# Optimization experiments

Measured on AMD Instinct MI355X. Metric: run time of the kernel, lower is better.

Reference implementation:

```python
import jax, jax.numpy as jnp
import numpy as np

B, T, D = 4, 2048, 1024
H, K, V, S, C = 8, 128, 128, 512, 256
R = T // C
W = 2 * C
TAU = float(K) ** 0.5
NEG = 1e30  # INFTY_APPROX from source


def rel_shift(x):
    # Transformer-XL relative shift; x: [B,H,R,C,W]
    lead = x.shape[:-2]
    c, w = x.shape[-2:]
    x = jnp.pad(x, [(0, 0)] * (x.ndim - 1) + [(1, 0)])
    x = x.reshape(*lead, w + 1, c)
    return x[..., 1:, :].reshape(*lead, c, w)


def setup_inputs():
    key = jax.random.key(0)
    ks = jax.random.split(key, 9)
    sd = lambda n: 1.0 / np.sqrt(n)
    f32 = jnp.float32
    return dict(
        x=jax.random.normal(ks[0], (B, T, D), f32),
        g_ln=jnp.ones((D,), f32),
        Wq=jax.random.normal(ks[1], (D, H, K), f32) * sd(D),
        Wk=jax.random.normal(ks[2], (D, H, K), f32) * sd(D),
        Wv=jax.random.normal(ks[3], (D, H, V), f32) * sd(D),
        codebook=jax.random.normal(ks[4], (H, S, K), f32),
        xl_r=jax.random.normal(ks[5], (H, W, K), f32) * sd(D),
        xl_u=jax.random.normal(ks[6], (H, K), f32) * 0.02,
        xl_v=jax.random.normal(ks[7], (H, K), f32) * 0.02,
        Wo=jax.random.normal(ks[8], (H, V, D), f32) * sd(H * V),
    )


def reference(x, g_ln, Wq, Wk, Wv, codebook, xl_r, xl_u, xl_v, Wo):
    # RMSNorm
    xt = x * jax.lax.rsqrt(jnp.mean(jnp.square(x), axis=-1, keepdims=True) + 1e-6) * g_ln
    # QKV projections, reshaped to blocks: [B,H,R,C,*]
    q = jnp.einsum('btd,dhk->bhtk', xt, Wq).reshape(B, H, R, C, K)
    k = jnp.einsum('btd,dhk->bhtk', xt, Wk).reshape(B, H, R, C, K)
    v = jnp.einsum('btd,dhv->bhtv', xt, Wv).reshape(B, H, R, C, V)
    # VQ codebook assignment (per-head nearest codeword)
    d2 = (jnp.sum(k * k, -1, keepdims=True)
          - 2.0 * jnp.einsum('bhrck,hsk->bhrcs', k, codebook)
          + jnp.sum(codebook * codebook, -1)[None, :, None, None, :])
    z = jnp.argmin(d2, axis=-1)                      # shortcodes [B,H,R,C]
    delta = jax.nn.one_hot(z, S, dtype=k.dtype)      # [B,H,R,C,S]
    k_hat_q = jnp.einsum('bhrcs,hsk->bhrck', delta, codebook)
    k_hat = k + jax.lax.stop_gradient(k_hat_q - k)   # straight-through quantized keys
    # causal cumulative per-code cluster stats ('matmul' reduction from source)
    d1 = jnp.sum(delta, axis=3)                      # counts per block [B,H,R,S]
    d1c = jnp.cumsum(d1, axis=2)
    fracs = jnp.tril(jnp.einsum('bhrs,bhgs->bhsrg', 1.0 / jnp.clip(d1c, 1.0), d1))
    lower = jnp.pad(d1c[:, :, :-2], ((0, 0), (0, 0), (2, 0), (0, 0)))
    dv = jnp.einsum('bhrcs,bhrcv->bhrsv', delta, v)
    dvn = dv / jnp.clip(d1[..., None], 1.0)
    dvnc = jnp.einsum('bhsrg,bhgsv->bhrsv', fracs, dvn)
    upper_div_lower = jnp.pad(dvnc[:, :, :-2], ((0, 0), (0, 0), (2, 0), (0, 0), (0, 0)))
    # attention over recent window (prev+current block) and codebook cache
    q_u = q + xl_u[None, :, None, None, :]
    q_v = q + xl_v[None, :, None, None, :]
    k_hat_prev = jnp.pad(k_hat[:, :, :-1], ((0, 0), (0, 0), (1, 0), (0, 0), (0, 0)))
    v_prev = jnp.pad(v[:, :, :-1], ((0, 0), (0, 0), (1, 0), (0, 0), (0, 0)))
    k_recent = jnp.concatenate([k_hat_prev, k_hat], axis=3)  # [B,H,R,W,K]
    v_recent = jnp.concatenate([v_prev, v], axis=3)          # [B,H,R,W,V]
    ac = jnp.einsum('bhrck,bhrwk->bhrcw', q_u, k_recent)
    bd = rel_shift(jnp.einsum('bhrck,hwk->bhrcw', q_v, xl_r))
    recent = (ac + bd) / TAU
    i = jnp.arange(C)[:, None]
    j = jnp.arange(W)[None, :]
    causal = j <= i + C                                            # [C,W]
    first = (jnp.arange(R)[:, None, None] == 0) & (j[None] < C)    # mask zero-padded prev of block 0
    mask = causal[None] & jnp.logical_not(first)                   # [R,C,W]
    recent = jnp.where(mask[None, None], recent, -NEG)
    cache = jnp.einsum('bhrck,hsk->bhrcs', q_u, codebook) / TAU
    cache = cache + jnp.where(lower > 0, jnp.log(jnp.maximum(lower, 1.0)), -NEG)[:, :, :, None, :]
    attn = jax.nn.softmax(jnp.concatenate([cache, recent], axis=-1), axis=-1)
    out = (jnp.einsum('bhrcs,bhrsv->bhrcv', attn[..., :S], upper_div_lower)
           + jnp.einsum('bhrcw,bhrwv->bhrcv', attn[..., S:], v_recent))
    res = jnp.einsum('bhtv,hvd->btd', out.reshape(B, H, T, V), Wo)
    return res
```

## Files before the change

### kernel.cpp

```cpp
#include <hip/hip_runtime.h>
#include <hip/hip_fp16.h>

typedef _Float16 half8 __attribute__((ext_vector_type(8)));
typedef float f32x4 __attribute__((ext_vector_type(4)));

constexpr int Bn = 4, Tn = 2048, Dn = 1024, Hn = 8, Kn = 128, Vn = 128;
constexpr int Sn = 512, Cn = 256, Rn = 8, Wn = 512;
constexpr float NEGV = 1.0e30f;
constexpr float INV_TAU = 0.08838834764831845f;

__device__ __forceinline__ half8 ldh8(const __half* p) {
  return *reinterpret_cast<const half8*>(p);
}
__device__ __forceinline__ void sth8(__half* p, half8 v) {
  *reinterpret_cast<half8*>(p) = v;
}
__device__ __forceinline__ f32x4 mfma16(half8 a, half8 b, f32x4 c) {
  return __builtin_amdgcn_mfma_f32_16x16x32_f16(a, b, c, 0, 0, 0);
}

__global__ __launch_bounds__(256) void rms3_k(const float* __restrict__ x,
                                              const float* __restrict__ g,
                                              __half* __restrict__ xth,
                                              __half* __restrict__ xtl) {
  const int row = blockIdx.x;
  const int tid = threadIdx.x;
  const float4 v = reinterpret_cast<const float4*>(x + (size_t)row * Dn)[tid];
  float ss = v.x * v.x + v.y * v.y + v.z * v.z + v.w * v.w;
#pragma unroll
  for (int o = 32; o > 0; o >>= 1) ss += __shfl_xor(ss, o);
  __shared__ float red[4];
  if ((tid & 63) == 0) red[tid >> 6] = ss;
  __syncthreads();
  const float tot = red[0] + red[1] + red[2] + red[3];
  const float sc = rsqrtf(tot * (1.0f / Dn) + 1e-6f);
  const float4 gv = reinterpret_cast<const float4*>(g)[tid];
  float vv[4] = {v.x * sc * gv.x, v.y * sc * gv.y, v.z * sc * gv.z,
                 v.w * sc * gv.w};
  __half hi[4], lo[4];
#pragma unroll
  for (int e = 0; e < 4; ++e) {
    hi[e] = __float2half(vv[e]);
    lo[e] = __float2half(vv[e] - __half2float(hi[e]));
  }
  __half2* oph = reinterpret_cast<__half2*>(xth + (size_t)row * Dn + tid * 4);
  __half2* opl = reinterpret_cast<__half2*>(xtl + (size_t)row * Dn + tid * 4);
  oph[0] = __halves2half2(hi[0], hi[1]);
  oph[1] = __halves2half2(hi[2], hi[3]);
  opl[0] = __halves2half2(lo[0], lo[1]);
  opl[1] = __halves2half2(lo[2], lo[3]);
}

__global__ __launch_bounds__(256) void transcvt_k(const float* __restrict__ src,
                                                  __half* __restrict__ dst) {
  __shared__ float ts[32][33];
  const int bx = blockIdx.x, by = blockIdx.y;
  const int j = threadIdx.x & 31, i0 = threadIdx.x >> 5;
#pragma unroll
  for (int rr = 0; rr < 4; ++rr) {
    const int row = i0 + rr * 8;
    ts[row][j] = src[(size_t)(by * 32 + row) * 1024 + bx * 32 + j];
  }
  __syncthreads();
#pragma unroll
  for (int rr = 0; rr < 4; ++rr) {
    const int row = i0 + rr * 8;
    dst[(size_t)(bx * 32 + row) * 1024 + by * 32 + j] = __float2half(ts[j][row]);
  }
}

__global__ __launch_bounds__(256) void transcvt2_k(
    const float* __restrict__ src, __half* __restrict__ dh,
    __half* __restrict__ dl) {
  __shared__ float ts[32][33];
  const int bx = blockIdx.x, by = blockIdx.y;
  const int j = threadIdx.x & 31, i0 = threadIdx.x >> 5;
#pragma unroll
  for (int rr = 0; rr < 4; ++rr) {
    const int row = i0 + rr * 8;
    ts[row][j] = src[(size_t)(by * 32 + row) * 1024 + bx * 32 + j];
  }
  __syncthreads();
#pragma unroll
  for (int rr = 0; rr < 4; ++rr) {
    const int row = i0 + rr * 8;
    const float v = ts[j][row];
    const __half hi = __float2half(v);
    dh[(size_t)(bx * 32 + row) * 1024 + by * 32 + j] = hi;
    dl[(size_t)(bx * 32 + row) * 1024 + by * 32 + j] =
        __float2half(v - __half2float(hi));
  }
}

__global__ __launch_bounds__(256) void cb2_k(const float* __restrict__ cb,
                                             float* __restrict__ cb2v) {
  const int idx = blockIdx.x * 256 + threadIdx.x;
  const float4* rp = reinterpret_cast<const float4*>(cb + (size_t)idx * Kn);
  float ss = 0.f;
#pragma unroll 8
  for (int i = 0; i < Kn / 4; ++i) {
    const float4 v = rp[i];
    ss += v.x * v.x + v.y * v.y + v.z * v.z + v.w * v.w;
  }
  cb2v[idx] = ss;
}

__global__ __launch_bounds__(256) void cvt2_k(const float* __restrict__ cb,
                                              const float* __restrict__ xlr,
                                              __half* __restrict__ cbh,
                                              __half* __restrict__ cbl,
                                              __half* __restrict__ xlrh) {
  const int i = blockIdx.x * 256 + threadIdx.x;
  constexpr int NE = Hn * Sn * Kn;
  if (i < NE) {
    const float v = cb[i];
    const __half hi = __float2half(v);
    cbh[i] = hi;
    cbl[i] = __float2half(v - __half2float(hi));
  } else {
    xlrh[i - NE] = __float2half(xlr[i - NE]);
  }
}

__global__ __launch_bounds__(256) void duv_k(const float* __restrict__ xlr,
                                             const float* __restrict__ xlu,
                                             const float* __restrict__ xlv,
                                             float* __restrict__ duv) {
  const int h = blockIdx.x;
  const float* up = xlu + h * Kn;
  const float* vp = xlv + h * Kn;
  for (int j = threadIdx.x; j < Wn; j += 256) {
    const float* rp = xlr + ((size_t)h * Wn + j) * Kn;
    float s = 0.f;
#pragma unroll 8
    for (int d = 0; d < Kn; ++d) s = fmaf(vp[d] - up[d], rp[d], s);
    duv[h * Wn + j] = s;
  }
}

__global__ __launch_bounds__(256, 2) void kproj_k(
    const __half* __restrict__ Ah, const __half* __restrict__ Al,
    const __half* __restrict__ Bh, const __half* __restrict__ Bl,
    __half* __restrict__ Ch, __half* __restrict__ Cl, int M, int KD) {
  __shared__ __half AsH[128 * 72];
  __shared__ __half AsL[128 * 72];
  __shared__ __half BsH[128 * 72];
  __shared__ __half BsL[128 * 72];
  const int tid = threadIdx.x;
  const int lane = tid & 63, wq = tid >> 6;
  const int lrow = lane & 15, lk8 = (lane >> 4) << 3;
  const int m0 = blockIdx.x * 128, n0 = blockIdx.y * 128;
  const int srow = tid >> 2, spart = tid & 3;

  f32x4 acc[2][8];
#pragma unroll
  for (int mt = 0; mt < 2; ++mt)
#pragma unroll
    for (int nt = 0; nt < 8; ++nt) acc[mt][nt] = (f32x4){0.f, 0.f, 0.f, 0.f};

  for (int kt = 0; kt < KD; kt += 64) {
    __syncthreads();
#pragma unroll
    for (int hh = 0; hh < 2; ++hh) {
      const int row = srow + hh * 64;
      const size_t ao = (size_t)(m0 + row) * KD + kt + spart * 16;
      const size_t bo = (size_t)(n0 + row) * KD + kt + spart * 16;
      sth8(&AsH[row * 72 + spart * 16], ldh8(Ah + ao));
      sth8(&AsH[row * 72 + spart * 16 + 8], ldh8(Ah + ao + 8));
      sth8(&AsL[row * 72 + spart * 16], ldh8(Al + ao));
      sth8(&AsL[row * 72 + spart * 16 + 8], ldh8(Al + ao + 8));
      sth8(&BsH[row * 72 + spart * 16], ldh8(Bh + bo));
      sth8(&BsH[row * 72 + spart * 16 + 8], ldh8(Bh + bo + 8));
      sth8(&BsL[row * 72 + spart * 16], ldh8(Bl + bo));
      sth8(&BsL[row * 72 + spart * 16 + 8], ldh8(Bl + bo + 8));
    }
    __syncthreads();
#pragma unroll
    for (int ks = 0; ks < 2; ++ks) {
      const half8 a0h = ldh8(&AsH[(32 * wq + lrow) * 72 + lk8 + 32 * ks]);
      const half8 a1h = ldh8(&AsH[(32 * wq + 16 + lrow) * 72 + lk8 + 32 * ks]);
      const half8 a0l = ldh8(&AsL[(32 * wq + lrow) * 72 + lk8 + 32 * ks]);
      const half8 a1l = ldh8(&AsL[(32 * wq + 16 + lrow) * 72 + lk8 + 32 * ks]);
#pragma unroll
      for (int nt = 0; nt < 8; ++nt) {
        const half8 bh = ldh8(&BsH[(16 * nt + lrow) * 72 + lk8 + 32 * ks]);
        const half8 bl = ldh8(&BsL[(16 * nt + lrow) * 72 + lk8 + 32 * ks]);
        acc[0][nt] = mfma16(a0h, bh, acc[0][nt]);
        acc[0][nt] = mfma16(a0h, bl, acc[0][nt]);
        acc[0][nt] = mfma16(a0l, bh, acc[0][nt]);
        acc[1][nt] = mfma16(a1h, bh, acc[1][nt]);
        acc[1][nt] = mfma16(a1h, bl, acc[1][nt]);
        acc[1][nt] = mfma16(a1l, bh, acc[1][nt]);
      }
    }
  }
  __half* OH = Ch + (size_t)(n0 >> 7) * M * 128;
  __half* OL = Cl + (size_t)(n0 >> 7) * M * 128;
#pragma unroll
  for (int mt = 0; mt < 2; ++mt)
#pragma unroll
    for (int nt = 0; nt < 8; ++nt)
#pragma unroll
      for (int reg = 0; reg < 4; ++reg) {
        const int row = m0 + 32 * wq + 16 * mt + 4 * (lane >> 4) + reg;
        const float v = acc[mt][nt][reg];
        const __half hi = __float2half(v);
        OH[(size_t)row * 128 + 16 * nt + lrow] = hi;
        OL[(size_t)row * 128 + 16 * nt + lrow] =
            __float2half(v - __half2float(hi));
      }
}

template <int MODE>
__global__ __launch_bounds__(256, 4) void gemmh_k(const __half* __restrict__ A,
                                                  const __half* __restrict__ Bt,
                                                  void* __restrict__ Cout,
                                                  int M, int N, int KD) {
  __shared__ __half As[128 * 72];
  __shared__ __half Bs[128 * 72];
  const int tid = threadIdx.x;
  const int lane = tid & 63, wq = tid >> 6;
  const int lrow = lane & 15, lk8 = (lane >> 4) << 3;
  const int m0 = blockIdx.x * 128, n0 = blockIdx.y * 128;
  const int srow = tid >> 2, spart = tid & 3;

  f32x4 acc[2][8];
#pragma unroll
  for (int mt = 0; mt < 2; ++mt)
#pragma unroll
    for (int nt = 0; nt < 8; ++nt) acc[mt][nt] = (f32x4){0.f, 0.f, 0.f, 0.f};

  for (int kt = 0; kt < KD; kt += 64) {
    __syncthreads();
#pragma unroll
    for (int hh = 0; hh < 2; ++hh) {
      const int row = srow + hh * 64;
      const __half* pa = A + (size_t)(m0 + row) * KD + kt + spart * 16;
      const __half* pb = Bt + (size_t)(n0 + row) * KD + kt + spart * 16;
      sth8(&As[row * 72 + spart * 16], ldh8(pa));
      sth8(&As[row * 72 + spart * 16 + 8], ldh8(pa + 8));
      sth8(&Bs[row * 72 + spart * 16], ldh8(pb));
      sth8(&Bs[row * 72 + spart * 16 + 8], ldh8(pb + 8));
    }
    __syncthreads();
#pragma unroll
    for (int ks = 0; ks < 2; ++ks) {
      half8 a0 = ldh8(&As[(32 * wq + lrow) * 72 + lk8 + 32 * ks]);
      half8 a1 = ldh8(&As[(32 * wq + 16 + lrow) * 72 + lk8 + 32 * ks]);
#pragma unroll
      for (int nt = 0; nt < 8; ++nt) {
        half8 b = ldh8(&Bs[(16 * nt + lrow) * 72 + lk8 + 32 * ks]);
        acc[0][nt] = mfma16(a0, b, acc[0][nt]);
        acc[1][nt] = mfma16(a1, b, acc[1][nt]);
      }
    }
  }
  if (MODE == 0) {
    __half* O = reinterpret_cast<__half*>(Cout) + (size_t)(n0 >> 7) * M * 128;
#pragma unroll
    for (int mt = 0; mt < 2; ++mt)
#pragma unroll
      for (int nt = 0; nt < 8; ++nt)
#pragma unroll
        for (int reg = 0; reg < 4; ++reg) {
          const int row = m0 + 32 * wq + 16 * mt + 4 * (lane >> 4) + reg;
          O[(size_t)row * 128 + 16 * nt + lrow] = __float2half(acc[mt][nt][reg]);
        }
  } else {
    float* O = reinterpret_cast<float*>(Cout);
#pragma unroll
    for (int mt = 0; mt < 2; ++mt)
#pragma unroll
      for (int nt = 0; nt < 8; ++nt)
#pragma unroll
        for (int reg = 0; reg < 4; ++reg) {
          const int row = m0 + 32 * wq + 16 * mt + 4 * (lane >> 4) + reg;
          O[(size_t)row * N + n0 + 16 * nt + lrow] = acc[mt][nt][reg];
        }
  }
}

__global__ __launch_bounds__(256, 2) void argmin3_k(
    const __half* __restrict__ kbh, const __half* __restrict__ kbl,
    const __half* __restrict__ cbh, const __half* __restrict__ cbl,
    const float* __restrict__ cb2v, int* __restrict__ zb) {
  __shared__ __half BsH[64 * 136];
  __shared__ __half BsL[64 * 136];
  const int tid = threadIdx.x;
  const int lane = tid & 63, wq = tid >> 6;
  const int lrow = lane & 15, lk8 = (lane >> 4) << 3;
  const int m0 = blockIdx.x * 128;
  const int h = blockIdx.y;
  const int srow = tid >> 2, spart = tid & 3;
  const size_t kbase = (size_t)h * (Bn * Tn);

  half8 ah[2][4], al[2][4];
#pragma unroll
  for (int mt = 0; mt < 2; ++mt)
#pragma unroll
    for (int ks = 0; ks < 4; ++ks) {
      const size_t off =
          (kbase + m0 + 32 * wq + 16 * mt + lrow) * 128 + lk8 + 32 * ks;
      ah[mt][ks] = ldh8(kbh + off);
      al[mt][ks] = ldh8(kbl + off);
    }

  float best[2][4];
  int bidx[2][4];
#pragma unroll
  for (int mt = 0; mt < 2; ++mt)
#pragma unroll
    for (int reg = 0; reg < 4; ++reg) {
      best[mt][reg] = 3.0e38f;
      bidx[mt][reg] = 0;
    }

  for (int s0 = 0; s0 < Sn; s0 += 64) {
    __syncthreads();
    {
      const size_t bo = ((size_t)h * Sn + s0 + srow) * 128 + spart * 32;
      sth8(&BsH[srow * 136 + spart * 32], ldh8(cbh + bo));
      sth8(&BsH[srow * 136 + spart * 32 + 8], ldh8(cbh + bo + 8));
      sth8(&BsH[srow * 136 + spart * 32 + 16], ldh8(cbh + bo + 16));
      sth8(&BsH[srow * 136 + spart * 32 + 24], ldh8(cbh + bo + 24));
      sth8(&BsL[srow * 136 + spart * 32], ldh8(cbl + bo));
      sth8(&BsL[srow * 136 + spart * 32 + 8], ldh8(cbl + bo + 8));
      sth8(&BsL[srow * 136 + spart * 32 + 16], ldh8(cbl + bo + 16));
      sth8(&BsL[srow * 136 + spart * 32 + 24], ldh8(cbl + bo + 24));
    }
    __syncthreads();
    f32x4 acc[2][4];
#pragma unroll
    for (int mt = 0; mt < 2; ++mt)
#pragma unroll
      for (int nt = 0; nt < 4; ++nt) acc[mt][nt] = (f32x4){0.f, 0.f, 0.f, 0.f};
#pragma unroll
    for (int ks = 0; ks < 4; ++ks)
#pragma unroll
      for (int nt = 0; nt < 4; ++nt) {
        const half8 bh = ldh8(&BsH[(16 * nt + lrow) * 136 + lk8 + 32 * ks]);
        const half8 bl = ldh8(&BsL[(16 * nt + lrow) * 136 + lk8 + 32 * ks]);
        acc[0][nt] = mfma16(ah[0][ks], bh, acc[0][nt]);
        acc[0][nt] = mfma16(ah[0][ks], bl, acc[0][nt]);
        acc[0][nt] = mfma16(al[0][ks], bh, acc[0][nt]);
        acc[1][nt] = mfma16(ah[1][ks], bh, acc[1][nt]);
        acc[1][nt] = mfma16(ah[1][ks], bl, acc[1][nt]);
        acc[1][nt] = mfma16(al[1][ks], bh, acc[1][nt]);
      }
#pragma unroll
    for (int mt = 0; mt < 2; ++mt)
#pragma unroll
      for (int nt = 0; nt < 4; ++nt) {
        const int s = s0 + 16 * nt + lrow;
        const float c2 = cb2v[h * Sn + s];
#pragma unroll
        for (int reg = 0; reg < 4; ++reg) {
          const float d2 = c2 - 2.0f * acc[mt][nt][reg];
          if (d2 < best[mt][reg]) {
            best[mt][reg] = d2;
            bidx[mt][reg] = s;
          }
        }
      }
  }
#pragma unroll
  for (int xb = 1; xb <= 8; xb <<= 1) {
#pragma unroll
    for (int mt = 0; mt < 2; ++mt)
#pragma unroll
      for (int reg = 0; reg < 4; ++reg) {
        const float ob = __shfl_xor(best[mt][reg], xb);
        const int oi = __shfl_xor(bidx[mt][reg], xb);
        if (ob < best[mt][reg] ||
            (ob == best[mt][reg] && oi < bidx[mt][reg])) {
          best[mt][reg] = ob;
          bidx[mt][reg] = oi;
        }
      }
  }
  if (lrow == 0) {
#pragma unroll
    for (int mt = 0; mt < 2; ++mt)
#pragma unroll
      for (int reg = 0; reg < 4; ++reg) {
        const int row = m0 + 32 * wq + 16 * mt + 4 * (lane >> 4) + reg;
        zb[kbase + row] = bidx[mt][reg];
      }
  }
}

__global__ __launch_bounds__(1024) void scan2_k(const int* __restrict__ zb,
                                                const __half* __restrict__ vb,
                                                __half* __restrict__ udl,
                                                float* __restrict__ biasv) {
  __shared__ float acc[64][128];
  __shared__ float cnt[64];
  const int tid = threadIdx.x;
  const int sc = blockIdx.x, b = blockIdx.y, h = blockIdx.z;
  const int s0 = sc * 64;
  for (int i = tid; i < 64 * 128; i += 1024) acc[i >> 7][i & 127] = 0.f;
  if (tid < 64) cnt[tid] = 0.f;
  __syncthreads();
  const size_t tokH = (size_t)h * (Bn * Tn) + (size_t)b * Tn;
  const int dd = tid & 127, slice = tid >> 7;
  for (int r = 0; r < Rn; ++r) {
    for (int i = tid; i < 64 * 128; i += 1024) {
      const int srow = i >> 7, d = i & 127;
      const float c = cnt[srow];
      udl[((((size_t)h * Bn + b) * Rn + r) * Sn + s0 + srow) * Vn + d] =
          __float2half(acc[srow][d] / fmaxf(c, 1.f));
    }
    if (tid < 64) {
      const float c = cnt[tid];
      biasv[(((size_t)h * Bn + b) * Rn + r) * Sn + s0 + tid] =
          (c > 0.f) ? logf(c) : -NEGV;
    }
    __syncthreads();
    if (r >= 1 && r < 7) {
      const int tb = (r - 1) * Cn;
#pragma unroll 4
      for (int u = 0; u < 32; ++u) {
        const int tok = tb + u * 8 + slice;
        const int s = zb[tokH + tok];
        if (s >= s0 && s < s0 + 64) {
          const float v = __half2float(vb[(tokH + tok) * Vn + dd]);
          atomicAdd(&acc[s - s0][dd], v);
          if (dd == 0) atomicAdd(&cnt[s - s0], 1.0f);
        }
      }
    }
    __syncthreads();
  }
}

__global__ __launch_bounds__(512, 2) void attn5_k(
    const __half* __restrict__ qbh, const __half* __restrict__ vbh,
    const __half* __restrict__ udl, const __half* __restrict__ cbh,
    const __half* __restrict__ xlrh, const float* __restrict__ biasv,
    const float* __restrict__ duv, const int* __restrict__ zb,
    const float* __restrict__ xlu, __half* __restrict__ aout) {
  __shared__ __half XS[320 * 136];
  __shared__ __half KS[64 * 136];
  __shared__ __half VtS[128 * 72];
  __shared__ __half Ebuf[8 * 16 * 82];

  const int tid = threadIdx.x;
  const int lane = tid & 63, wq = tid >> 6;
  const int lrow = lane & 15, hi = lane >> 4, lk8 = hi << 3;
  const int bx = blockIdx.x;
  const int b = bx >> 3, r = bx & 7;
  const int h = blockIdx.y;
  const int cm0 = 32 * wq;
  const size_t tokH = (size_t)h * (Bn * Tn) + (size_t)b * Tn;
  const size_t sBase = (((size_t)h * Bn + b) * Rn + r) * Sn;
  const int tBlk = r * Cn;
  __half* Ew = &Ebuf[wq * 16 * 82];
  __half* Pw = &XS[(40 * wq) * 136];

  half8 a[2][4];
#pragma unroll
  for (int mt = 0; mt < 2; ++mt) {
    const size_t qrow = (tokH + tBlk + cm0 + 16 * mt + lrow) * Kn;
#pragma unroll
    for (int ks = 0; ks < 4; ++ks) {
      const int col = lk8 + 32 * ks;
      half8 q = ldh8(qbh + qrow + col);
      const float* up = xlu + h * Kn + col;
      half8 t;
#pragma unroll
      for (int e = 0; e < 8; ++e) t[e] = (_Float16)((float)q[e] + up[e]);
      a[mt][ks] = t;
    }
  }

  float mR[2][4], lR[2][4];
  f32x4 Oacc[2][8];
#pragma unroll
  for (int mt = 0; mt < 2; ++mt) {
#pragma unroll
    for (int i = 0; i < 4; ++i) {
      mR[mt][i] = -NEGV;
      lR[mt][i] = 0.f;
    }
#pragma unroll
    for (int nt = 0; nt < 8; ++nt) Oacc[mt][nt] = (f32x4){0.f, 0.f, 0.f, 0.f};
  }

  const int krow = tid >> 3, kpart = tid & 7;
  const int kp = tid >> 4, p16 = tid & 15;

  for (int ch = 0; ch < 16; ++ch) {
    const bool isC = (ch < 8);
    const int s0 = ch * 64;
    const int w0 = (ch - 8) * 64;
    __syncthreads();
    if (isC) {
      {
        const __half* ks = cbh + ((size_t)h * Sn + s0 + krow) * Kn + kpart * 16;
        sth8(&KS[krow * 136 + kpart * 16], ldh8(ks));
        sth8(&KS[krow * 136 + kpart * 16 + 8], ldh8(ks + 8));
      }
      {
        const __half* u0 = udl + (sBase + s0 + 2 * kp) * Vn + p16 * 8;
        const __half* u1 = u0 + Vn;
#pragma unroll
        for (int e = 0; e < 8; ++e) {
          const int d = p16 * 8 + e;
          const int gidx = ((2 * kp) >> 3) ^ ((d >> 4) & 7);
          *reinterpret_cast<__half2*>(
              &VtS[d * 72 + gidx * 8 + ((2 * kp) & 7)]) =
              __halves2half2(u0[e], u1[e]);
        }
      }
    } else {
      {
        int tk = (r - 1) * Cn + w0 + krow;
        if (tk < 0) tk = 0;
        const int code = zb[tokH + tk];
        const __half* ks = cbh + ((size_t)h * Sn + code) * Kn + kpart * 16;
        sth8(&KS[krow * 136 + kpart * 16], ldh8(ks));
        sth8(&KS[krow * 136 + kpart * 16 + 8], ldh8(ks + 8));
      }
      {
        const int tk0 = (r - 1) * Cn + w0 + 2 * kp;
        const int tka = tk0 < 0 ? 0 : tk0;
        const int tkb = tk0 + 1 < 0 ? 0 : tk0 + 1;
        const __half* v0 = vbh + (tokH + tka) * Kn + p16 * 8;
        const __half* v1 = vbh + (tokH + tkb) * Kn + p16 * 8;
#pragma unroll
        for (int e = 0; e < 8; ++e) {
          const int d = p16 * 8 + e;
          const int gidx = ((2 * kp) >> 3) ^ ((d >> 4) & 7);
          *reinterpret_cast<__half2*>(
              &VtS[d * 72 + gidx * 8 + ((2 * kp) & 7)]) =
              __halves2half2(v0[e], v1[e]);
        }
      }
      for (int jl = tid >> 1; jl < 320; jl += 256) {
        const int p2 = tid & 1;
        int j = w0 + jl;
        j = j > Wn - 1 ? Wn - 1 : j;
        const __half* xs = xlrh + ((size_t)h * Wn + j) * Kn + 64 * p2;
        __half* xd = &XS[jl * 136 + 64 * p2];
#pragma unroll
        for (int g8 = 0; g8 < 8; ++g8) sth8(xd + 8 * g8, ldh8(xs + 8 * g8));
      }
    }
    __syncthreads();

    f32x4 acc[2][4];
#pragma unroll
    for (int mt = 0; mt < 2; ++mt)
#pragma unroll
      for (int nt = 0; nt < 4; ++nt) acc[mt][nt] = (f32x4){0.f, 0.f, 0.f, 0.f};
#pragma unroll
    for (int ks = 0; ks < 4; ++ks) {
#pragma unroll
      for (int nt = 0; nt < 4; ++nt) {
        const half8 bfr = ldh8(&KS[(16 * nt + lrow) * 136 + lk8 + 32 * ks]);
        acc[0][nt] = mfma16(a[0][ks], bfr, acc[0][nt]);
        acc[1][nt] = mfma16(a[1][ks], bfr, acc[1][nt]);
      }
    }

    float lg[2][4][4];
    if (isC) {
#pragma unroll
      for (int nt = 0; nt < 4; ++nt) {
        const float bv = biasv[sBase + s0 + 16 * nt + lrow];
#pragma unroll
        for (int mt = 0; mt < 2; ++mt)
#pragma unroll
          for (int reg = 0; reg < 4; ++reg)
            lg[mt][nt][reg] = acc[mt][nt][reg] * INV_TAU + bv;
      }
    } else {
#pragma unroll
      for (int mt = 0; mt < 2; ++mt) {
        const int cmt = cm0 + 16 * mt;
        const int bbase = 240 - cmt;
        f32x4 eacc[5];
#pragma unroll
        for (int nt = 0; nt < 5; ++nt) eacc[nt] = (f32x4){0.f, 0.f, 0.f, 0.f};
#pragma unroll
        for (int ks = 0; ks < 4; ++ks)
#pragma unroll
          for (int nt = 0; nt < 5; ++nt)
            eacc[nt] = mfma16(
                a[mt][ks],
                ldh8(&XS[(bbase + 16 * nt + lrow) * 136 + lk8 + 32 * ks]),
                eacc[nt]);
#pragma unroll
        for (int nt = 0; nt < 5; ++nt) {
          int j = w0 + bbase + 16 * nt + lrow;
          j = j > Wn - 1 ? Wn - 1 : j;
          const float dv = duv[h * Wn + j];
#pragma unroll
          for (int reg = 0; reg < 4; ++reg)
            Ew[(4 * hi + reg) * 82 + 16 * nt + lrow] =
                __float2half(eacc[nt][reg] + dv);
        }
#pragma unroll
        for (int nt = 0; nt < 4; ++nt) {
          const int kw = 16 * nt + lrow;
          const int w = w0 + kw;
#pragma unroll
          for (int reg = 0; reg < 4; ++reg) {
            const int cl = 4 * hi + reg;
            const int cabs = cmt + cl;
            const bool valid = (w <= cabs + Cn) && !(r == 0 && w < Cn);
            const float bdv = __half2float(Ew[cl * 82 + kw + 15 - cl]);
            lg[mt][nt][reg] =
                valid ? (acc[mt][nt][reg] + bdv) * INV_TAU : -NEGV;
          }
        }
      }
    }
    float p[2][4][4];
#pragma unroll
    for (int mt = 0; mt < 2; ++mt) {
#pragma unroll
      for (int reg = 0; reg < 4; ++reg) {
        float rm = fmaxf(fmaxf(lg[mt][0][reg], lg[mt][1][reg]),
                         fmaxf(lg[mt][2][reg], lg[mt][3][reg]));
        rm = fmaxf(rm, __shfl_xor(rm, 1));
        rm = fmaxf(rm, __shfl_xor(rm, 2));
        rm = fmaxf(rm, __shfl_xor(rm, 4));
        rm = fmaxf(rm, __shfl_xor(rm, 8));
        const float mn = fmaxf(mR[mt][reg], rm);
        const float scl = __expf(mR[mt][reg] - mn);
        float rs = 0.f;
#pragma unroll
        for (int nt = 0; nt < 4; ++nt) {
          p[mt][nt][reg] = __expf(lg[mt][nt][reg] - mn);
          rs += p[mt][nt][reg];
        }
        rs += __shfl_xor(rs, 1);
        rs += __shfl_xor(rs, 2);
        rs += __shfl_xor(rs, 4);
        rs += __shfl_xor(rs, 8);
        lR[mt][reg] = lR[mt][reg] * scl + rs;
        mR[mt][reg] = mn;
#pragma unroll
        for (int nt = 0; nt < 8; ++nt) Oacc[mt][nt][reg] *= scl;
      }
    }
    if (!isC) __syncthreads();
#pragma unroll
    for (int mt = 0; mt < 2; ++mt)
#pragma unroll
      for (int nt = 0; nt < 4; ++nt)
#pragma unroll
        for (int reg = 0; reg < 4; ++reg)
          Pw[(16 * mt + 4 * hi + reg) * 136 + lrow + 16 * nt] =
              __float2half(p[mt][nt][reg]);
#pragma unroll
    for (int ks = 0; ks < 2; ++ks) {
#pragma unroll
      for (int mt = 0; mt < 2; ++mt) {
        const half8 pa = ldh8(&Pw[(16 * mt + lrow) * 136 + lk8 + 32 * ks]);
#pragma unroll
        for (int nt = 0; nt < 8; ++nt) {
          const int gidx = (((lk8 + 32 * ks) >> 3) ^ nt);
          const half8 vv = ldh8(&VtS[(16 * nt + lrow) * 72 + gidx * 8]);
          Oacc[mt][nt] = mfma16(pa, vv, Oacc[mt][nt]);
        }
      }
    }
  }
#pragma unroll
  for (int mt = 0; mt < 2; ++mt) {
    float inv[4];
#pragma unroll
    for (int reg = 0; reg < 4; ++reg) inv[reg] = 1.0f / lR[mt][reg];
#pragma unroll
    for (int nt = 0; nt < 8; ++nt)
#pragma unroll
      for (int reg = 0; reg < 4; ++reg) {
        const int c = cm0 + 16 * mt + 4 * hi + reg;
        aout[((size_t)b * Tn + tBlk + c) * (Hn * Vn) + h * Vn + 16 * nt +
             lrow] = __float2half(Oacc[mt][nt][reg] * inv[reg]);
      }
  }
}

extern "C" void kernel_launch(void* const* d_in, const int* in_sizes, int n_in,
                              void* d_out, int out_size, void* d_ws,
                              size_t ws_size, hipStream_t stream) {
  (void)in_sizes;
  (void)n_in;
  (void)out_size;
  const float* x = (const float*)d_in[0];
  const float* g_ln = (const float*)d_in[1];
  const float* Wq = (const float*)d_in[2];
  const float* Wk = (const float*)d_in[3];
  const float* Wv = (const float*)d_in[4];
  const float* cb = (const float*)d_in[5];
  const float* xl_r = (const float*)d_in[6];
  const float* xl_u = (const float*)d_in[7];
  const float* xl_v = (const float*)d_in[8];
  const float* Wo = (const float*)d_in[9];
  float* out = (float*)d_out;

  float* W = (float*)d_ws;
  size_t o = 0;
  __half* xth = (__half*)(W + o);
  __half* aout = xth;
  o += (size_t)Bn * Tn * Dn / 2;
  __half* xtl = (__half*)(W + o);
  o += (size_t)Bn * Tn * Dn / 2;
  __half* kbh = (__half*)(W + o);
  __half* udlh = kbh;
  o += (size_t)Hn * Bn * Tn * Kn / 2;
  __half* kbl = (__half*)(W + o);
  o += (size_t)Hn * Bn * Tn * Kn / 2;
  __half* qbh = (__half*)(W + o);
  o += (size_t)Hn * Bn * Tn * Kn / 2;
  __half* vbh = (__half*)(W + o);
  o += (size_t)Hn * Bn * Tn * Vn / 2;
  __half* cbh = (__half*)(W + o);
  o += (size_t)Hn * Sn * Kn / 2;
  __half* cbl = (__half*)(W + o);
  o += (size_t)Hn * Sn * Kn / 2;
  __half* xlrh = (__half*)(W + o);
  o += (size_t)Hn * Wn * Kn / 2;
  int* zb = (int*)(W + o);
  o += (size_t)Hn * Bn * Tn;
  float* biasb = W + o;
  o += (size_t)Hn * Bn * Rn * Sn;
  float* duvb = W + o;
  o += (size_t)Hn * Wn;
  float* cb2b = W + o;
  o += (size_t)Hn * Sn;
  __half* wkth = (__half*)(W + o);
  o += (size_t)Dn * Dn / 2;
  __half* wktl = (__half*)(W + o);
  o += (size_t)Dn * Dn / 2;
  __half* wqt = (__half*)(W + o);
  o += (size_t)Dn * Dn / 2;
  __half* wvt = (__half*)(W + o);
  o += (size_t)Dn * Dn / 2;
  __half* wot = (__half*)(W + o);
  o += (size_t)Dn * Dn / 2;

  if (ws_size < o * sizeof(float)) return;

  rms3_k<<<Bn * Tn, 256, 0, stream>>>(x, g_ln, xth, xtl);
  transcvt2_k<<<dim3(32, 32), 256, 0, stream>>>(Wk, wkth, wktl);
  transcvt_k<<<dim3(32, 32), 256, 0, stream>>>(Wq, wqt);
  transcvt_k<<<dim3(32, 32), 256, 0, stream>>>(Wv, wvt);
  transcvt_k<<<dim3(32, 32), 256, 0, stream>>>(Wo, wot);
  cb2_k<<<Hn * Sn / 256, 256, 0, stream>>>(cb, cb2b);
  cvt2_k<<<2 * Hn * Sn * Kn / 256, 256, 0, stream>>>(cb, xl_r, cbh, cbl, xlrh);
  duv_k<<<Hn, 256, 0, stream>>>(xl_r, xl_u, xl_v, duvb);

  kproj_k<<<dim3(64, 8), 256, 0, stream>>>(xth, xtl, wkth, wktl, kbh, kbl,
                                           8192, 1024);
  gemmh_k<0><<<dim3(64, 8), 256, 0, stream>>>(xth, wqt, qbh, 8192, 1024, 1024);
  gemmh_k<0><<<dim3(64, 8), 256, 0, stream>>>(xth, wvt, vbh, 8192, 1024, 1024);

  argmin3_k<<<dim3(Bn * Tn / 128, Hn), 256, 0, stream>>>(kbh, kbl, cbh, cbl,
                                                         cb2b, zb);
  scan2_k<<<dim3(8, Bn, Hn), 1024, 0, stream>>>(zb, vbh, udlh, biasb);

  attn5_k<<<dim3(Bn * Rn, Hn), 512, 0, stream>>>(
      qbh, vbh, udlh, cbh, xlrh, biasb, duvb, zb, xl_u, aout);

  gemmh_k<1><<<dim3(64, 8), 256, 0, stream>>>(aout, wot, out, 8192, 1024,
                                              1024);
}
```

Baseline: 396.4 us.

## Merge weight transposes, skip empty cache chunks, shuffle-based rel-shift in attention

The four weight transpose/convert launches become one 3D-grid kernel. The attention kernel skips cache chunks for the early blocks whose cumulative code statistics are empty (r==0 starts at the second half of the recent chunks, r==1 skips the cache), and caches the duv bias in shared memory. The rel-shift now uses cross-lane shuffles instead of a per-wave LDS staging buffer. P moves to its own LDS buffer so one barrier can be dropped, at the cost of extra shared memory and possible occupancy pressure.

After: 418.3 us. +5.5%, slower.

```diff
diff --git a/kernel.cpp b/kernel.cpp
--- a/kernel.cpp
+++ b/kernel.cpp
@@ -51,9 +51,15 @@
   opl[1] = __halves2half2(lo[2], lo[3]);
 }
 
-__global__ __launch_bounds__(256) void transcvt_k(const float* __restrict__ src,
-                                                  __half* __restrict__ dst) {
+__global__ __launch_bounds__(256) void transall_k(
+    const float* __restrict__ Wq, const float* __restrict__ Wv,
+    const float* __restrict__ Wo, const float* __restrict__ Wk,
+    __half* __restrict__ wqt, __half* __restrict__ wvt,
+    __half* __restrict__ wot, __half* __restrict__ wkth,
+    __half* __restrict__ wktl) {
   __shared__ float ts[32][33];
+  const int z = blockIdx.z;
+  const float* src = (z == 0) ? Wq : (z == 1) ? Wv : (z == 2) ? Wo : Wk;
   const int bx = blockIdx.x, by = blockIdx.y;
   const int j = threadIdx.x & 31, i0 = threadIdx.x >> 5;
 #pragma unroll
@@ -62,33 +68,24 @@
     ts[row][j] = src[(size_t)(by * 32 + row) * 1024 + bx * 32 + j];
   }
   __syncthreads();
-#pragma unroll
-  for (int rr = 0; rr < 4; ++rr) {
-    const int row = i0 + rr * 8;
-    dst[(size_t)(bx * 32 + row) * 1024 + by * 32 + j] = __float2half(ts[j][row]);
-  }
-}
-
-__global__ __launch_bounds__(256) void transcvt2_k(
-    const float* __restrict__ src, __half* __restrict__ dh,
-    __half* __restrict__ dl) {
-  __shared__ float ts[32][33];
-  const int bx = blockIdx.x, by = blockIdx.y;
-  const int j = threadIdx.x & 31, i0 = threadIdx.x >> 5;
-#pragma unroll
-  for (int rr = 0; rr < 4; ++rr) {
-    const int row = i0 + rr * 8;
-    ts[row][j] = src[(size_t)(by * 32 + row) * 1024 + bx * 32 + j];
-  }
-  __syncthreads();
-#pragma unroll
-  for (int rr = 0; rr < 4; ++rr) {
-    const int row = i0 + rr * 8;
-    const float v = ts[j][row];
-    const __half hi = __float2half(v);
-    dh[(size_t)(bx * 32 + row) * 1024 + by * 32 + j] = hi;
-    dl[(size_t)(bx * 32 + row) * 1024 + by * 32 + j] =
-        __float2half(v - __half2float(hi));
+  if (z < 3) {
+    __half* dst = (z == 0) ? wqt : (z == 1) ? wvt : wot;
+#pragma unroll
+    for (int rr = 0; rr < 4; ++rr) {
+      const int row = i0 + rr * 8;
+      dst[(size_t)(bx * 32 + row) * 1024 + by * 32 + j] =
+          __float2half(ts[j][row]);
+    }
+  } else {
+#pragma unroll
+    for (int rr = 0; rr < 4; ++rr) {
+      const int row = i0 + rr * 8;
+      const float v = ts[j][row];
+      const __half hi = __float2half(v);
+      wkth[(size_t)(bx * 32 + row) * 1024 + by * 32 + j] = hi;
+      wktl[(size_t)(bx * 32 + row) * 1024 + by * 32 + j] =
+          __float2half(v - __half2float(hi));
+    }
   }
 }
 
@@ -433,7 +430,7 @@
   }
 }
 
-__global__ __launch_bounds__(512, 2) void attn5_k(
+__global__ __launch_bounds__(512, 2) void attn6_k(
     const __half* __restrict__ qbh, const __half* __restrict__ vbh,
     const __half* __restrict__ udl, const __half* __restrict__ cbh,
     const __half* __restrict__ xlrh, const float* __restrict__ biasv,
@@ -442,7 +439,8 @@
   __shared__ __half XS[320 * 136];
   __shared__ __half KS[64 * 136];
   __shared__ __half VtS[128 * 72];
-  __shared__ __half Ebuf[8 * 16 * 82];
+  __shared__ __half PS[8 * 32 * 72];
+  __shared__ float duvS[320];
 
   const int tid = threadIdx.x;
   const int lane = tid & 63, wq = tid >> 6;
@@ -454,8 +452,7 @@
   const size_t tokH = (size_t)h * (Bn * Tn) + (size_t)b * Tn;
   const size_t sBase = (((size_t)h * Bn + b) * Rn + r) * Sn;
   const int tBlk = r * Cn;
-  __half* Ew = &Ebuf[wq * 16 * 82];
-  __half* Pw = &XS[(40 * wq) * 136];
+  __half* Pw = &PS[wq * 32 * 72];
 
   half8 a[2][4];
 #pragma unroll
@@ -489,7 +486,9 @@
   const int krow = tid >> 3, kpart = tid & 7;
   const int kp = tid >> 4, p16 = tid & 15;
 
-  for (int ch = 0; ch < 16; ++ch) {
+  const int chStart = (r >= 2) ? 0 : ((r == 1) ? 8 : 12);
+
+  for (int ch = chStart; ch < 16; ++ch) {
     const bool isC = (ch < 8);
     const int s0 = ch * 64;
     const int w0 = (ch - 8) * 64;
@@ -545,6 +544,11 @@
 #pragma unroll
         for (int g8 = 0; g8 < 8; ++g8) sth8(xd + 8 * g8, ldh8(xs + 8 * g8));
       }
+      for (int jl = tid; jl < 320; jl += 512) {
+        int j = w0 + jl;
+        j = j > Wn - 1 ? Wn - 1 : j;
+        duvS[jl] = duv[h * Wn + j];
+      }
     }
     __syncthreads();
 
@@ -592,24 +596,25 @@
                 eacc[nt]);
 #pragma unroll
         for (int nt = 0; nt < 5; ++nt) {
-          int j = w0 + bbase + 16 * nt + lrow;
-          j = j > Wn - 1 ? Wn - 1 : j;
-          const float dv = duv[h * Wn + j];
-#pragma unroll
-          for (int reg = 0; reg < 4; ++reg)
-            Ew[(4 * hi + reg) * 82 + 16 * nt + lrow] =
-                __float2half(eacc[nt][reg] + dv);
-        }
-#pragma unroll
-        for (int nt = 0; nt < 4; ++nt) {
-          const int kw = 16 * nt + lrow;
-          const int w = w0 + kw;
-#pragma unroll
-          for (int reg = 0; reg < 4; ++reg) {
-            const int cl = 4 * hi + reg;
+          const float dv = duvS[bbase + 16 * nt + lrow];
+#pragma unroll
+          for (int reg = 0; reg < 4; ++reg) eacc[nt][reg] += dv;
+        }
+#pragma unroll
+        for (int reg = 0; reg < 4; ++reg) {
+          const int cl = 4 * hi + reg;
+          const int t = lrow + 15 - cl;
+          const int src = (lane & 48) | (t & 15);
+          float val[5];
+#pragma unroll
+          for (int n5 = 0; n5 < 5; ++n5) val[n5] = __shfl(eacc[n5][reg], src);
+          const bool selhi = (t & 16) != 0;
+#pragma unroll
+          for (int nt = 0; nt < 4; ++nt) {
+            const float bdv = selhi ? val[nt + 1] : val[nt];
+            const int w = w0 + 16 * nt + lrow;
             const int cabs = cmt + cl;
             const bool valid = (w <= cabs + Cn) && !(r == 0 && w < Cn);
-            const float bdv = __half2float(Ew[cl * 82 + kw + 15 - cl]);
             lg[mt][nt][reg] =
                 valid ? (acc[mt][nt][reg] + bdv) * INV_TAU : -NEGV;
           }
@@ -645,20 +650,19 @@
         for (int nt = 0; nt < 8; ++nt) Oacc[mt][nt][reg] *= scl;
       }
     }
-    if (!isC) __syncthreads();
 #pragma unroll
     for (int mt = 0; mt < 2; ++mt)
 #pragma unroll
       for (int nt = 0; nt < 4; ++nt)
 #pragma unroll
         for (int reg = 0; reg < 4; ++reg)
-          Pw[(16 * mt + 4 * hi + reg) * 136 + lrow + 16 * nt] =
+          Pw[(16 * mt + 4 * hi + reg) * 72 + lrow + 16 * nt] =
               __float2half(p[mt][nt][reg]);
 #pragma unroll
     for (int ks = 0; ks < 2; ++ks) {
 #pragma unroll
       for (int mt = 0; mt < 2; ++mt) {
-        const half8 pa = ldh8(&Pw[(16 * mt + lrow) * 136 + lk8 + 32 * ks]);
+        const half8 pa = ldh8(&Pw[(16 * mt + lrow) * 72 + lk8 + 32 * ks]);
 #pragma unroll
         for (int nt = 0; nt < 8; ++nt) {
           const int gidx = (((lk8 + 32 * ks) >> 3) ^ nt);
@@ -746,10 +750,8 @@
   if (ws_size < o * sizeof(float)) return;
 
   rms3_k<<<Bn * Tn, 256, 0, stream>>>(x, g_ln, xth, xtl);
-  transcvt2_k<<<dim3(32, 32), 256, 0, stream>>>(Wk, wkth, wktl);
-  transcvt_k<<<dim3(32, 32), 256, 0, stream>>>(Wq, wqt);
-  transcvt_k<<<dim3(32, 32), 256, 0, stream>>>(Wv, wvt);
-  transcvt_k<<<dim3(32, 32), 256, 0, stream>>>(Wo, wot);
+  transall_k<<<dim3(32, 32, 4), 256, 0, stream>>>(Wq, Wv, Wo, Wk, wqt, wvt,
+                                                  wot, wkth, wktl);
   cb2_k<<<Hn * Sn / 256, 256, 0, stream>>>(cb, cb2b);
   cvt2_k<<<2 * Hn * Sn * Kn / 256, 256, 0, stream>>>(cb, xl_r, cbh, cbl, xlrh);
   duv_k<<<Hn, 256, 0, stream>>>(xl_r, xl_u, xl_v, duvb);
@@ -763,7 +765,7 @@
                                                          cb2b, zb);
   scan2_k<<<dim3(8, Bn, Hn), 1024, 0, stream>>>(zb, vbh, udlh, biasb);
 
-  attn5_k<<<dim3(Bn * Rn, Hn), 512, 0, stream>>>(
+  attn6_k<<<dim3(Bn * Rn, Hn), 512, 0, stream>>>(
       qbh, vbh, udlh, cbh, xlrh, biasb, duvb, zb, xl_u, aout);
 
   gemmh_k<1><<<dim3(64, 8), 256, 0, stream>>>(aout, wot, out, 8192, 1024,
```
